# Performance work log

Measured on AMD Instinct MI355X. Metric: run time of the kernel, lower is better.

Reference implementation:

```python
import jax, jax.numpy as jnp
import numpy as np

GAMMA = 0.99
ENTROPY_COEF = 0.01
GAE_LAMBDA = 0.95
VALUE_LOSS_COEF = 0.5

T = 65536          # agent rollout length
O, S, A = 8, 1048576, 6  # opponents, steps, actions


def setup_inputs() -> dict:
    key = jax.random.key(0)
    ks = jax.random.split(key, 9)
    return {
        "agent_rewards": jax.random.normal(ks[0], (T,), jnp.float32),
        "agent_log_probs": jax.random.normal(ks[1], (T,), jnp.float32),
        "agent_values": jax.random.normal(ks[2], (T + 1,), jnp.float32),
        "agent_entropies": jax.random.uniform(ks[3], (T,), jnp.float32),
        "opponent_log_probs": jax.random.normal(ks[4], (O, S, A), jnp.float32),
        "opponent_actions_ground_truths": jax.random.randint(ks[5], (O, S), 0, A),
        "opponent_values": jax.random.normal(ks[6], (O, S), jnp.float32),
        "opponent_rewards": jax.random.normal(ks[7], (O, S - 1), jnp.float32),
        "opponent_coefs": jax.random.uniform(ks[8], (O,), jnp.float32),
    }


def _agent_loss(rewards, values, log_probs, entropies):
    # Sequential GAE / discounted-return recurrence, scanned from last step to first.
    def step(carry, xs):
        R, gae, pl, vl = carry
        r, v, v_next, lp, ent = xs
        R = GAMMA * R + r
        adv = R - v
        vl = vl + 0.5 * adv * adv
        delta = r + GAMMA * v_next - v
        gae = gae * GAMMA * GAE_LAMBDA + delta
        pl = pl - lp * jax.lax.stop_gradient(gae) - ENTROPY_COEF * ent
        return (R, gae, pl, vl), None

    init = (values[-1], jnp.float32(0.0), jnp.float32(0.0), jnp.float32(0.0))
    xs = (rewards, values[:-1], values[1:], log_probs, entropies)
    (_, _, pl, vl), _ = jax.lax.scan(step, init, xs, reverse=True)
    return pl + VALUE_LOSS_COEF * vl


def _opponent_loss(log_probs, actions, values, rewards, coefs):
    # cross_entropy in torch applies log_softmax to its input, even though the arg
    # is (mis)named log_probs -> ce = mean(logsumexp(logits) - logits[target])
    logZ = jax.nn.logsumexp(log_probs, axis=-1)                      # (O, S)
    tgt = jnp.take_along_axis(log_probs, actions[..., None], axis=-1)[..., 0]
    ce = jnp.mean(logZ - tgt, axis=-1)                               # (O,)
    policy_loss = coefs * ce

    v0 = values[:, :-1]                                              # (O, S-1)
    v_next = values[:, 1:]                                           # roll(-1) then truncate
    pred = rewards + GAMMA * v_next
    d = v0 - pred
    ad = jnp.abs(d)
    sl1 = jnp.mean(jnp.where(ad < 1.0, 0.5 * d * d, ad - 0.5), axis=-1)
    value_loss = coefs * sl1
    return jnp.sum(policy_loss + value_loss)


def reference(agent_rewards, agent_log_probs, agent_values, agent_entropies,
              opponent_log_probs, opponent_actions_ground_truths,
              opponent_values, opponent_rewards, opponent_coefs):
    agent_loss = _agent_loss(agent_rewards, agent_values, agent_log_probs, agent_entropies)
    opp_loss = _opponent_loss(opponent_log_probs, opponent_actions_ground_truths,
                              opponent_values, opponent_rewards, opponent_coefs)
    return jnp.sum(agent_loss + opp_loss)
```

## Files before the change

### kernel.cpp

```cpp
#include <hip/hip_runtime.h>
#include <cstddef>

constexpr float GAMMA = 0.99f;
constexpr float GLAM  = 0.99f * 0.95f;
constexpr float ENT_C = 0.01f;

constexpr int T = 65536;
constexpr int O = 8;
constexpr int S = 1048576;
constexpr int A = 6;
constexpr int BLK = 256;

constexpr int BPO        = 512;
constexpr int OPP_BLOCKS = O * BPO;
constexpr int ROWS_PER_B = S / BPO;
constexpr int ROWS_PER_T = ROWS_PER_B / BLK;
constexpr int CHUNK = T / BLK;


__global__ __launch_bounds__(BLK)
void fused_kernel(const float* __restrict__ arew,
                  const float* __restrict__ alp,
                  const float* __restrict__ aval,
                  const float* __restrict__ aent,
                  const float* __restrict__ olp,
                  const int*   __restrict__ oact,
                  const float* __restrict__ oval,
                  const float* __restrict__ orew,
                  float* __restrict__ ws)
{
    const int tid = threadIdx.x;

    if (blockIdx.x == 0) {
        __shared__ float sR[BLK], sG[BLK];
        const int base = tid * CHUNK;

        float cR = 0.f, cG = 0.f;
        float nextv = aval[base + CHUNK];
        #pragma unroll 4
        for (int k4 = CHUNK - 4; k4 >= 0; k4 -= 4) {
            float4 r4 = *reinterpret_cast<const float4*>(&arew[base + k4]);
            float4 v4 = *reinterpret_cast<const float4*>(&aval[base + k4]);
            cR = GAMMA * cR + r4.w;  cG = GLAM * cG + (r4.w + GAMMA * nextv - v4.w);
            cR = GAMMA * cR + r4.z;  cG = GLAM * cG + (r4.z + GAMMA * v4.w  - v4.z);
            cR = GAMMA * cR + r4.y;  cG = GLAM * cG + (r4.y + GAMMA * v4.z  - v4.y);
            cR = GAMMA * cR + r4.x;  cG = GLAM * cG + (r4.x + GAMMA * v4.y  - v4.x);
            nextv = v4.x;
        }
        sR[tid] = cR; sG[tid] = cG;
        __syncthreads();

        if (tid == 0) {
            double aRd = 1.0, aGd = 1.0;
            for (int i = 0; i < CHUNK; ++i) { aRd *= 0.99; aGd *= 0.99 * 0.95; }
            const float aR = (float)aRd, aG = (float)aGd;
            float Rin = aval[T];
            float Gin = 0.f;
            for (int i = BLK - 1; i >= 0; --i) {
                float cr = sR[i], cg = sG[i];
                sR[i] = Rin; sG[i] = Gin;
                Rin = aR * Rin + cr;
                Gin = aG * Gin + cg;
            }
        }
        __syncthreads();
        float R = sR[tid], g = sG[tid];
        __syncthreads();

        float pl = 0.f, vl = 0.f;
        nextv = aval[base + CHUNK];
        #pragma unroll 4
        for (int k4 = CHUNK - 4; k4 >= 0; k4 -= 4) {
            float4 r4 = *reinterpret_cast<const float4*>(&arew[base + k4]);
            float4 v4 = *reinterpret_cast<const float4*>(&aval[base + k4]);
            float4 l4 = *reinterpret_cast<const float4*>(&alp [base + k4]);
            float4 e4 = *reinterpret_cast<const float4*>(&aent[base + k4]);

            R = GAMMA * R + r4.w; { float adv = R - v4.w; vl += 0.5f * adv * adv; }
            g = GLAM * g + (r4.w + GAMMA * nextv - v4.w); pl += -l4.w * g - ENT_C * e4.w;
            R = GAMMA * R + r4.z; { float adv = R - v4.z; vl += 0.5f * adv * adv; }
            g = GLAM * g + (r4.z + GAMMA * v4.w  - v4.z); pl += -l4.z * g - ENT_C * e4.z;
            R = GAMMA * R + r4.y; { float adv = R - v4.y; vl += 0.5f * adv * adv; }
            g = GLAM * g + (r4.y + GAMMA * v4.z  - v4.y); pl += -l4.y * g - ENT_C * e4.y;
            R = GAMMA * R + r4.x; { float adv = R - v4.x; vl += 0.5f * adv * adv; }
            g = GLAM * g + (r4.x + GAMMA * v4.y  - v4.x); pl += -l4.x * g - ENT_C * e4.x;
            nextv = v4.x;
        }
        sR[tid] = pl; sG[tid] = vl;
        __syncthreads();
        for (int stp = BLK / 2; stp > 0; stp >>= 1) {
            if (tid < stp) { sR[tid] += sR[tid + stp]; sG[tid] += sG[tid + stp]; }
            __syncthreads();
        }
        if (tid == 0) ws[2 * OPP_BLOCKS] = sR[0] + 0.5f * sG[0];
        return;
    }

    const int bid = blockIdx.x - 1;
    const int o   = bid / BPO;
    const int seg = bid % BPO;
    const int row0 = seg * ROWS_PER_B;

    float ce_acc = 0.f, sl_acc = 0.f;

    #pragma unroll
    for (int it = 0; it < ROWS_PER_T / 4; ++it) {
        const int srel = row0 + it * (BLK * 4) + tid * 4;
        const size_t gr = (size_t)o * S + srel;

        const float* lp = olp + gr * (size_t)A;
        float4 q0 = reinterpret_cast<const float4*>(lp)[0];
        float4 q1 = reinterpret_cast<const float4*>(lp)[1];
        float4 q2 = reinterpret_cast<const float4*>(lp)[2];
        float4 q3 = reinterpret_cast<const float4*>(lp)[3];
        float4 q4 = reinterpret_cast<const float4*>(lp)[4];
        float4 q5 = reinterpret_cast<const float4*>(lp)[5];
        int4 act = *reinterpret_cast<const int4*>(&oact[gr]);

        float lg[24] = { q0.x,q0.y,q0.z,q0.w, q1.x,q1.y,q1.z,q1.w,
                         q2.x,q2.y,q2.z,q2.w, q3.x,q3.y,q3.z,q3.w,
                         q4.x,q4.y,q4.z,q4.w, q5.x,q5.y,q5.z,q5.w };
        int ac[4] = { act.x, act.y, act.z, act.w };
        #pragma unroll
        for (int j = 0; j < 4; ++j) {
            const float* l = &lg[6 * j];
            float m = fmaxf(fmaxf(fmaxf(l[0], l[1]), fmaxf(l[2], l[3])), fmaxf(l[4], l[5]));
            float se = __expf(l[0]-m) + __expf(l[1]-m) + __expf(l[2]-m)
                     + __expf(l[3]-m) + __expf(l[4]-m) + __expf(l[5]-m);
            ce_acc += (m + __logf(se)) - l[ac[j]];
        }

        float4 v4 = *reinterpret_cast<const float4*>(&oval[gr]);
        float v[5] = { v4.x, v4.y, v4.z, v4.w,
                       (srel + 4 <= S - 1) ? oval[gr + 4] : 0.f };
        const size_t rr = (size_t)o * (S - 1) + srel;
        #pragma unroll
        for (int j = 0; j < 4; ++j) {
            if (srel + j < S - 1) {
                float rw = orew[rr + j];
                float d  = v[j] - (rw + GAMMA * v[j + 1]);
                float ad = fabsf(d);
                sl_acc += (ad < 1.f) ? 0.5f * d * d : ad - 0.5f;
            }
        }
    }

    __shared__ float s1[BLK], s2[BLK];
    s1[tid] = ce_acc; s2[tid] = sl_acc;
    __syncthreads();
    for (int stp = BLK / 2; stp > 0; stp >>= 1) {
        if (tid < stp) { s1[tid] += s1[tid + stp]; s2[tid] += s2[tid + stp]; }
        __syncthreads();
    }
    if (tid == 0) {
        ws[bid]              = s1[0];
        ws[OPP_BLOCKS + bid] = s2[0];
    }
}

__global__ __launch_bounds__(BLK)
void finalize_kernel(const float* __restrict__ ws,
                     const float* __restrict__ coefs,
                     float* __restrict__ out)
{
    const int tid = threadIdx.x;
    __shared__ float r1[BLK], r2[BLK];
    float tot = 0.f;
    for (int o = 0; o < O; ++o) {
        const float* cw = ws + o * BPO;
        const float* sw = ws + OPP_BLOCKS + o * BPO;
        r1[tid] = cw[tid] + cw[tid + BLK];
        r2[tid] = sw[tid] + sw[tid + BLK];
        __syncthreads();
        for (int stp = BLK / 2; stp > 0; stp >>= 1) {
            if (tid < stp) { r1[tid] += r1[tid + stp]; r2[tid] += r2[tid + stp]; }
            __syncthreads();
        }
        if (tid == 0)
            tot += coefs[o] * (r1[0] / (float)S + r2[0] / (float)(S - 1));
        __syncthreads();
    }
    if (tid == 0) out[0] = tot + ws[2 * OPP_BLOCKS];
}

extern "C" void kernel_launch(void* const* d_in, const int* in_sizes, int n_in,
                              void* d_out, int out_size, void* d_ws, size_t ws_size,
                              hipStream_t stream)
{
    const float* arew  = (const float*)d_in[0];
    const float* alp   = (const float*)d_in[1];
    const float* aval  = (const float*)d_in[2];
    const float* aent  = (const float*)d_in[3];
    const float* olp   = (const float*)d_in[4];
    const int*   oact  = (const int*)  d_in[5];
    const float* oval  = (const float*)d_in[6];
    const float* orew  = (const float*)d_in[7];
    const float* ocoef = (const float*)d_in[8];
    float* ws = (float*)d_ws;

    fused_kernel<<<1 + OPP_BLOCKS, BLK, 0, stream>>>(arew, alp, aval, aent,
                                                     olp, oact, oval, orew, ws);
    finalize_kernel<<<1, BLK, 0, stream>>>(ws, ocoef, (float*)d_out);
}
```

Before: 107.7 us.

## Stage opponent logits through LDS with coalesced loads and register prefetch

Replaces the per-thread strided 96-byte logit reads with coalesced float4 loads of a 512-row tile into shared memory, from which each thread reads two rows. The next stage's loads are issued into registers before the current tile is processed, so global latency overlaps compute. Target selection uses a select chain instead of dynamic indexing into a local array, which avoids scratch memory. The cost is two block barriers per stage and fewer rows in flight per thread.

```diff
diff --git a/kernel.cpp b/kernel.cpp
--- a/kernel.cpp
+++ b/kernel.cpp
@@ -14,9 +14,21 @@
 constexpr int BPO        = 512;
 constexpr int OPP_BLOCKS = O * BPO;
 constexpr int ROWS_PER_B = S / BPO;
-constexpr int ROWS_PER_T = ROWS_PER_B / BLK;
-constexpr int CHUNK = T / BLK;
-
+constexpr int STAGE_ROWS = 512;
+constexpr int NSTAGE     = ROWS_PER_B / STAGE_ROWS;
+constexpr int CHUNK      = T / BLK;
+
+
+__device__ __forceinline__ float row_ce(float l0, float l1, float l2,
+                                        float l3, float l4, float l5, int a)
+{
+    float m  = fmaxf(fmaxf(fmaxf(l0, l1), fmaxf(l2, l3)), fmaxf(l4, l5));
+    float se = __expf(l0 - m) + __expf(l1 - m) + __expf(l2 - m) +
+               __expf(l3 - m) + __expf(l4 - m) + __expf(l5 - m);
+    float tgt = (a == 0) ? l0 : (a == 1) ? l1 : (a == 2) ? l2 :
+                (a == 3) ? l3 : (a == 4) ? l4 : l5;
+    return (m + __logf(se)) - tgt;
+}
 
 __global__ __launch_bounds__(BLK)
 void fused_kernel(const float* __restrict__ arew,
@@ -30,9 +42,9 @@
                   float* __restrict__ ws)
 {
     const int tid = threadIdx.x;
+    __shared__ float s1[BLK], s2[BLK];
 
     if (blockIdx.x == 0) {
-        __shared__ float sR[BLK], sG[BLK];
         const int base = tid * CHUNK;
 
         float cR = 0.f, cG = 0.f;
@@ -47,7 +59,7 @@
             cR = GAMMA * cR + r4.x;  cG = GLAM * cG + (r4.x + GAMMA * v4.y  - v4.x);
             nextv = v4.x;
         }
-        sR[tid] = cR; sG[tid] = cG;
+        s1[tid] = cR; s2[tid] = cG;
         __syncthreads();
 
         if (tid == 0) {
@@ -57,14 +69,14 @@
             float Rin = aval[T];
             float Gin = 0.f;
             for (int i = BLK - 1; i >= 0; --i) {
-                float cr = sR[i], cg = sG[i];
-                sR[i] = Rin; sG[i] = Gin;
+                float cr = s1[i], cg = s2[i];
+                s1[i] = Rin; s2[i] = Gin;
                 Rin = aR * Rin + cr;
                 Gin = aG * Gin + cg;
             }
         }
         __syncthreads();
-        float R = sR[tid], g = sG[tid];
+        float R = s1[tid], g = s2[tid];
         __syncthreads();
 
         float pl = 0.f, vl = 0.f;
@@ -86,66 +98,78 @@
             g = GLAM * g + (r4.x + GAMMA * v4.y  - v4.x); pl += -l4.x * g - ENT_C * e4.x;
             nextv = v4.x;
         }
-        sR[tid] = pl; sG[tid] = vl;
+        s1[tid] = pl; s2[tid] = vl;
         __syncthreads();
         for (int stp = BLK / 2; stp > 0; stp >>= 1) {
-            if (tid < stp) { sR[tid] += sR[tid + stp]; sG[tid] += sG[tid + stp]; }
+            if (tid < stp) { s1[tid] += s1[tid + stp]; s2[tid] += s2[tid + stp]; }
             __syncthreads();
         }
-        if (tid == 0) ws[2 * OPP_BLOCKS] = sR[0] + 0.5f * sG[0];
+        if (tid == 0) ws[2 * OPP_BLOCKS] = s1[0] + 0.5f * s2[0];
         return;
     }
 
-    const int bid = blockIdx.x - 1;
-    const int o   = bid / BPO;
-    const int seg = bid % BPO;
+    __shared__ float lds[STAGE_ROWS * A];
+
+    const int bid  = blockIdx.x - 1;
+    const int o    = bid / BPO;
+    const int seg  = bid % BPO;
     const int row0 = seg * ROWS_PER_B;
+    const size_t obase = (size_t)o * S;
+    const size_t rbase = (size_t)o * (S - 1);
+
+    float4 pa, pb, pc; int2 pact; float2 pv; float pv2, pr0, pr1;
+
+    auto issue = [&](int s) {
+        const int srow = row0 + s * STAGE_ROWS;
+        const float4* lp4 = reinterpret_cast<const float4*>(olp + (obase + srow) * (size_t)A);
+        pa = lp4[tid];
+        pb = lp4[tid + BLK];
+        pc = lp4[tid + 2 * BLK];
+        const int r = srow + 2 * tid;
+        const size_t gr = obase + r;
+        pact = *reinterpret_cast<const int2*>(&oact[gr]);
+        pv   = *reinterpret_cast<const float2*>(&oval[gr]);
+        pv2  = (r + 2 <= S - 1) ? oval[gr + 2] : 0.f;
+        pr0  = orew[rbase + r];
+        pr1  = (r + 1 < S - 1) ? orew[rbase + r + 1] : 0.f;
+    };
 
     float ce_acc = 0.f, sl_acc = 0.f;
+    issue(0);
 
     #pragma unroll
-    for (int it = 0; it < ROWS_PER_T / 4; ++it) {
-        const int srel = row0 + it * (BLK * 4) + tid * 4;
-        const size_t gr = (size_t)o * S + srel;
-
-        const float* lp = olp + gr * (size_t)A;
-        float4 q0 = reinterpret_cast<const float4*>(lp)[0];
-        float4 q1 = reinterpret_cast<const float4*>(lp)[1];
-        float4 q2 = reinterpret_cast<const float4*>(lp)[2];
-        float4 q3 = reinterpret_cast<const float4*>(lp)[3];
-        float4 q4 = reinterpret_cast<const float4*>(lp)[4];
-        float4 q5 = reinterpret_cast<const float4*>(lp)[5];
-        int4 act = *reinterpret_cast<const int4*>(&oact[gr]);
-
-        float lg[24] = { q0.x,q0.y,q0.z,q0.w, q1.x,q1.y,q1.z,q1.w,
-                         q2.x,q2.y,q2.z,q2.w, q3.x,q3.y,q3.z,q3.w,
-                         q4.x,q4.y,q4.z,q4.w, q5.x,q5.y,q5.z,q5.w };
-        int ac[4] = { act.x, act.y, act.z, act.w };
-        #pragma unroll
-        for (int j = 0; j < 4; ++j) {
-            const float* l = &lg[6 * j];
-            float m = fmaxf(fmaxf(fmaxf(l[0], l[1]), fmaxf(l[2], l[3])), fmaxf(l[4], l[5]));
-            float se = __expf(l[0]-m) + __expf(l[1]-m) + __expf(l[2]-m)
-                     + __expf(l[3]-m) + __expf(l[4]-m) + __expf(l[5]-m);
-            ce_acc += (m + __logf(se)) - l[ac[j]];
-        }
-
-        float4 v4 = *reinterpret_cast<const float4*>(&oval[gr]);
-        float v[5] = { v4.x, v4.y, v4.z, v4.w,
-                       (srel + 4 <= S - 1) ? oval[gr + 4] : 0.f };
-        const size_t rr = (size_t)o * (S - 1) + srel;
-        #pragma unroll
-        for (int j = 0; j < 4; ++j) {
-            if (srel + j < S - 1) {
-                float rw = orew[rr + j];
-                float d  = v[j] - (rw + GAMMA * v[j + 1]);
-                float ad = fabsf(d);
-                sl_acc += (ad < 1.f) ? 0.5f * d * d : ad - 0.5f;
-            }
-        }
-    }
-
-    __shared__ float s1[BLK], s2[BLK];
+    for (int s = 0; s < NSTAGE; ++s) {
+        __syncthreads();
+        reinterpret_cast<float4*>(lds)[tid]           = pa;
+        reinterpret_cast<float4*>(lds)[tid + BLK]     = pb;
+        reinterpret_cast<float4*>(lds)[tid + 2 * BLK] = pc;
+        const int2  act = pact;
+        const float2 v  = pv;
+        const float v2 = pv2, rw0 = pr0, rw1 = pr1;
+        const int r = row0 + s * STAGE_ROWS + 2 * tid;
+        if (s + 1 < NSTAGE) issue(s + 1);
+        __syncthreads();
+
+        const float* lrow = &lds[12 * tid];
+        float4 q0 = *reinterpret_cast<const float4*>(lrow);
+        float4 q1 = *reinterpret_cast<const float4*>(lrow + 4);
+        float4 q2 = *reinterpret_cast<const float4*>(lrow + 8);
+
+        ce_acc += row_ce(q0.x, q0.y, q0.z, q0.w, q1.x, q1.y, act.x);
+        ce_acc += row_ce(q1.z, q1.w, q2.x, q2.y, q2.z, q2.w, act.y);
+
+        {
+            float d  = v.x - (rw0 + GAMMA * v.y);
+            float ad = fabsf(d);
+            sl_acc += (ad < 1.f) ? 0.5f * d * d : ad - 0.5f;
+        }
+        if (r + 1 < S - 1) {
+            float d  = v.y - (rw1 + GAMMA * v2);
+            float ad = fabsf(d);
+            sl_acc += (ad < 1.f) ? 0.5f * d * d : ad - 0.5f;
+        }
+    }
+
     s1[tid] = ce_acc; s2[tid] = sl_acc;
     __syncthreads();
     for (int stp = BLK / 2; stp > 0; stp >>= 1) {
@@ -167,7 +191,7 @@
     __shared__ float r1[BLK], r2[BLK];
     float tot = 0.f;
     for (int o = 0; o < O; ++o) {
-        const float* cw = ws + o * BPO;
+        const float* cw = ws + o * (BPO);
         const float* sw = ws + OPP_BLOCKS + o * BPO;
         r1[tid] = cw[tid] + cw[tid + BLK];
         r2[tid] = sw[tid] + sw[tid + BLK];
```

After: 100.8 us. 1.07x faster.
